# Kernel tuning notes

Measured on AMD Instinct MI355X. Metric: run time of the kernel, lower is better.

The kernel has to match this reference:

```python
import jax, jax.numpy as jnp
import numpy as np
import math

B, L, T, IN, H, DEPTH, HEADS = 4096, 1, 64, 16, 128, 3, 2
HD = H // HEADS
EPS = 1e-5


def layer_norm(x, g, b):
    u = jnp.mean(x, axis=-1, keepdims=True)
    s = jnp.mean((x - u) ** 2, axis=-1, keepdims=True)
    return g * (x - u) / jnp.sqrt(s + EPS) + b


def mlp(x, W, b, g, beta):
    return jax.nn.relu(layer_norm(x @ W + b, g, beta))


def attention(h, amask, Wq, bq, Wk, bk, Wv, bv):
    N, Tn, _ = h.shape
    def heads(x):
        return x.reshape(N, Tn, HEADS, HD).transpose(0, 2, 1, 3)
    q = heads(h @ Wq + bq)
    k = heads(h @ Wk + bk)
    v = heads(h @ Wv + bv)
    scores = jnp.einsum('nhqd,nhkd->nhqk', q, k) / math.sqrt(HD)
    scores = scores + (1.0 - amask[:, None]) * -10000.0
    probs = jax.nn.softmax(scores, axis=-1)
    ctx = jnp.einsum('nhqk,nhkd->nhqd', probs, v)
    return ctx.transpose(0, 2, 1, 3).reshape(N, Tn, H)


def setup_inputs() -> dict:
    key = jax.random.key(0)
    ks = jax.random.split(key, 8)
    feat = jax.random.normal(ks[0], (B, L, T, IN), jnp.float32)
    seq_lens = jax.random.randint(ks[1], (B, L), 1, T + 1)
    pos = jnp.arange(T)
    # repo convention: 0 = valid node, 1 = padded; prefix-valid layout
    masks = (pos[None, None, :] >= seq_lens[..., None]).astype(jnp.float32)[..., None]
    s = 0.02
    W_emb = jax.random.normal(ks[2], (IN, H), jnp.float32) * s
    W_enc = jax.random.normal(ks[3], (H, H), jnp.float32) * s
    Wq = jax.random.normal(ks[4], (DEPTH, H, H), jnp.float32) * s
    Wk = jax.random.normal(ks[5], (DEPTH, H, H), jnp.float32) * s
    Wv = jax.random.normal(ks[6], (DEPTH, H, H), jnp.float32) * s
    return dict(
        lane_nodes_feat=feat, masks=masks,
        W_emb=W_emb, b_emb=jnp.zeros((H,)), g_emb=jnp.ones((H,)), beta_emb=jnp.zeros((H,)),
        W_enc=W_enc, b_enc=jnp.zeros((H,)), g_enc=jnp.ones((H,)), beta_enc=jnp.zeros((H,)),
        Wq=Wq, bq=jnp.zeros((DEPTH, H)), Wk=Wk, bk=jnp.zeros((DEPTH, H)), Wv=Wv, bv=jnp.zeros((DEPTH, H)),
        ln_g=jnp.ones((DEPTH, H)), ln_b=jnp.zeros((DEPTH, H)),
    )


def reference(lane_nodes_feat, masks, W_emb, b_emb, g_emb, beta_emb, W_enc, b_enc,
              g_enc, beta_enc, Wq, bq, Wk, bk, Wv, bv, ln_g, ln_b):
    emb = mlp(lane_nodes_feat, W_emb, b_emb, g_emb, beta_emb)   # [B,L,T,H]
    emb = mlp(emb, W_enc, b_enc, g_enc, beta_enc)
    # every (b,l) lane has >=1 valid node by construction, so masked_select == reshape
    hs = emb.reshape(B * L, T, H)
    seq_lens = jnp.sum(1.0 - masks[:, :, :, 0], axis=-1).reshape(B * L)  # [N]
    pos = jnp.arange(T)
    valid = pos[None, :] < seq_lens[:, None]                              # [N,T]
    amask = (valid[:, :, None] & valid[:, None, :]).astype(hs.dtype)      # [N,T,T]
    for d in range(DEPTH):
        temp = hs
        hs = attention(hs, amask, Wq[d], bq[d], Wk[d], bk[d], Wv[d], bv[d])
        hs = jax.nn.relu(hs) + temp
        hs = layer_norm(hs, ln_g[d], ln_b[d])
    hs = jnp.max(hs, axis=1)                                              # [N,H]
    return hs.reshape(B, L, H)
```

## Files before the change

kernel.cpp:

```cpp
#include <hip/hip_runtime.h>

typedef unsigned short u16;
typedef unsigned int u32;
typedef __attribute__((ext_vector_type(8))) short short8;
typedef __attribute__((ext_vector_type(4))) float floatx4;

#define EPSV 1e-5f
#define WS_ELEMS 167936

__device__ __forceinline__ float b2f(u16 u){
  union { float f; u32 i; } c; c.i = ((u32)u) << 16; return c.f;
}
__device__ __forceinline__ u16 f2b(float f){
  union { float f; u32 i; } c; c.f = f;
  u32 r = c.i + 0x7FFFu + ((c.i >> 16) & 1u);
  return (u16)(r >> 16);
}
__device__ __forceinline__ u16 f2bc(float f){
  union { float f; u32 i; } c; c.f = f;
  return (u16)((c.i + 0x8000u) >> 16);
}
__device__ __forceinline__ float ldf(const void* p, int i, bool isf){
  return isf ? ((const float*)p)[i] : b2f(((const u16*)p)[i]);
}
__device__ __forceinline__ bool detect_f32(const void* g_emb){
  return *(const u32*)g_emb == 0x3F800000u;
}
__device__ __forceinline__ void dma16(const u16* g, u16* l){
  __builtin_amdgcn_global_load_lds((const __attribute__((address_space(1))) u32*)(g),
                                   (__attribute__((address_space(3))) u32*)(l), 16, 0, 0);
}
__device__ __forceinline__ void dma_slab(const u16* g, u16* dst, int wave, int lane){
  #pragma unroll
  for (int i = 0; i < 4; i++){
    int c = (wave << 2) + i;
    dma16(g + (c << 9) + (lane << 3), dst + (c << 9));
  }
}

__global__ void prep_kernel(const void* W_emb, const void* W_enc,
                            const void* Wq, const void* Wk, const void* Wv,
                            const void* g_emb, u16* ws){
  bool isf = detect_f32(g_emb);
  int e = blockIdx.x * 256 + threadIdx.x;
  if (e >= WS_ELEMS) return;
  float v;
  if (e < 4096){
    int half = e >> 11, r = e & 2047;
    int nt = r >> 9, q = (r >> 3) & 63, j = r & 7;
    int col = half*64 + nt*16 + (q & 15);
    int k = (q >> 4)*8 + j;
    v = (k < 16) ? ldf(W_emb, k*128 + col, isf) : 0.0f;
  } else if (e < 20480){
    int i = e - 4096;
    int half = i >> 13, r = i & 8191;
    int chunk = r >> 9, q = (r >> 3) & 63, j = r & 7;
    int ks = chunk >> 2, nt = chunk & 3;
    int col = half*64 + nt*16 + (q & 15);
    int k = ks*32 + (q >> 4)*8 + j;
    v = ldf(W_enc, k*128 + col, isf);
  } else {
    int i = e - 20480;
    int slab = i >> 13, r = i & 8191;
    int dh = slab / 3, which = slab - dh*3;
    int d = dh >> 1, h = dh & 1;
    int chunk = r >> 9, q = (r >> 3) & 63, j = r & 7;
    int ks = chunk >> 2, nt = chunk & 3;
    int col = h*64 + nt*16 + (q & 15);
    int k = ks*32 + (q >> 4)*8 + j;
    const void* W = (which == 0) ? Wv : (which == 1) ? Wk : Wq;
    v = ldf(W, d*16384 + k*128 + col, isf);
  }
  ws[e] = f2b(v);
}

__device__ __forceinline__ short8 frg(const u16* p, int chunk, int lane){
  return *(const short8*)(p + (chunk << 9) + (lane << 3));
}
__device__ __forceinline__ int wfoff(int wave, int nt, int lq, int lc){
  return ((((nt >> 1) << 2) + wave) << 9)
       + ((((((nt << 1) + (lc >> 3)) & 3) << 4) + (lq << 2)) << 3) + (lc & 7);
}
__device__ __forceinline__ int qfoff(int wave, int nt, int lq, int lc){
  return (wave << 10) + ((nt >> 1) << 9)
       + ((((((nt << 1) + (lc >> 3)) & 3) << 4) + (lq << 2)) << 3) + (lc & 7);
}

__device__ __forceinline__ void gemmW(const u16* sh, const u16* slab, int wave, int lane, floatx4* acc){
  #pragma unroll
  for (int ks = 0; ks < 4; ks++){
    short8 a = frg(sh, ks*4 + wave, lane);
    #pragma unroll
    for (int nt = 0; nt < 4; nt++)
      acc[nt] = __builtin_amdgcn_mfma_f32_16x16x32_bf16(a, frg(slab, ks*4 + nt, lane), acc[nt], 0, 0, 0);
  }
}
__device__ __forceinline__ void gemmWT(const u16* sh, const u16* slab, int wave, int lane, floatx4* acc){
  #pragma unroll
  for (int ks = 0; ks < 4; ks++){
    short8 a = frg(slab, ks*4 + wave, lane);
    #pragma unroll
    for (int nt = 0; nt < 4; nt++)
      acc[nt] = __builtin_amdgcn_mfma_f32_16x16x32_bf16(a, frg(sh, ks*4 + nt, lane), acc[nt], 0, 0, 0);
  }
}
__device__ __forceinline__ void gemm64(const u16* areg, const u16* b, int wave, int lane, floatx4* acc){
  #pragma unroll
  for (int ks = 0; ks < 2; ks++){
    short8 a = *(const short8*)(areg + (wave << 10) + (ks << 9) + (lane << 3));
    #pragma unroll
    for (int nt = 0; nt < 4; nt++)
      acc[nt] = __builtin_amdgcn_mfma_f32_16x16x32_bf16(a, frg(b, ks*4 + nt, lane), acc[nt], 0, 0, 0);
  }
}

__device__ __forceinline__ void red_sum2(float* s1, float* s2){
  #pragma unroll
  for (int m = 1; m < 16; m <<= 1){
    #pragma unroll
    for (int r = 0; r < 4; r++){
      s1[r] += __shfl_xor(s1[r], m, 64);
      s2[r] += __shfl_xor(s2[r], m, 64);
    }
  }
}

__device__ __forceinline__ void ln_mlp(floatx4* acc, const void* bias, const void* g,
    const void* bet, bool isf, float xres[8][4], int wave, int lq, int lc, u16* sh){
  float x[8][4], s1[4] = {0,0,0,0}, s2[4] = {0,0,0,0};
  #pragma unroll
  for (int nt = 0; nt < 8; nt++){
    float bb = ldf(bias, nt*16 + lc, isf);
    #pragma unroll
    for (int r = 0; r < 4; r++){
      float v = acc[nt][r] + bb;
      x[nt][r] = v; s1[r] += v; s2[r] += v*v;
    }
  }
  red_sum2(s1, s2);
  float mean[4], rstd[4];
  #pragma unroll
  for (int r = 0; r < 4; r++){
    mean[r] = s1[r] * (1.0f/128.0f);
    rstd[r] = rsqrtf(s2[r]*(1.0f/128.0f) - mean[r]*mean[r] + EPSV);
  }
  #pragma unroll
  for (int nt = 0; nt < 8; nt++){
    float gg = ldf(g, nt*16 + lc, isf), bb = ldf(bet, nt*16 + lc, isf);
    int o = wfoff(wave, nt, lq, lc);
    #pragma unroll
    for (int r = 0; r < 4; r++){
      float y = fmaxf((x[nt][r] - mean[r]) * rstd[r] * gg + bb, 0.0f);
      xres[nt][r] = y;
      sh[o + 8*r] = f2bc(y);
    }
  }
}

__device__ __forceinline__ void ln_attn(floatx4* ctx, float xres[8][4], const u16* cb,
                                        int wave, int lq, int lc, u16* sh){
  float x[8][4], s1[4] = {0,0,0,0}, s2[4] = {0,0,0,0};
  #pragma unroll
  for (int nt = 0; nt < 8; nt++){
    #pragma unroll
    for (int r = 0; r < 4; r++){
      float v = fmaxf(ctx[nt][r], 0.0f) + xres[nt][r];
      x[nt][r] = v; s1[r] += v; s2[r] += v*v;
    }
  }
  red_sum2(s1, s2);
  float mean[4], rstd[4];
  #pragma unroll
  for (int r = 0; r < 4; r++){
    mean[r] = s1[r] * (1.0f/128.0f);
    rstd[r] = rsqrtf(s2[r]*(1.0f/128.0f) - mean[r]*mean[r] + EPSV);
  }
  #pragma unroll
  for (int nt = 0; nt < 8; nt++){
    float gg = b2f(cb[384 + nt*16 + lc]), bb = b2f(cb[512 + nt*16 + lc]);
    int o = wfoff(wave, nt, lq, lc);
    #pragma unroll
    for (int r = 0; r < 4; r++){
      float y = (x[nt][r] - mean[r]) * rstd[r] * gg + bb;
      xres[nt][r] = y;
      sh[o + 8*r] = f2bc(y);
    }
  }
}

__global__ __launch_bounds__(256, 3)
void fused_kernel(const void* feat, const void* masks,
                  const void* b_emb, const void* g_emb, const void* be_emb,
                  const void* b_enc, const void* g_enc, const void* be_enc,
                  const void* bq, const void* bk, const void* bv,
                  const void* ln_g, const void* ln_b,
                  const u16* ws, void* out){
  __shared__ __align__(16) u16 s_h[8192];
  __shared__ __align__(16) u16 s_w[8192];
  __shared__ __align__(16) u16 s_k[4096];
  __shared__ __align__(16) u16 s_v[4096];
  __shared__ u16 s_c[1920];
  __shared__ float s_valid[64];

  int tid = threadIdx.x;
  int wave = tid >> 6, lane = tid & 63, lq = lane >> 4, lc = lane & 15;
  int n = blockIdx.x;
  bool isf = detect_f32(g_emb);
  const floatx4 z4 = {0.0f, 0.0f, 0.0f, 0.0f};

  dma16(ws + ((wave*2 + 0) << 9) + (lane << 3), s_w + ((wave*2 + 0) << 9));
  dma16(ws + ((wave*2 + 1) << 9) + (lane << 3), s_w + ((wave*2 + 1) << 9));

  if (!isf){
    const u16* fp = (const u16*)feat + n*1024;
    if (tid < 128){
      int t = tid >> 1, half = tid & 1;
      uint4 v = *(const uint4*)(fp + t*16 + half*8);
      *(uint4*)(s_h + ((t >> 4) << 9) + (((half << 4) + (t & 15)) << 3)) = v;
    } else {
      int t = (tid - 128) >> 1, half = 2 + ((tid - 128) & 1);
      uint4 z; z.x = 0; z.y = 0; z.z = 0; z.w = 0;
      *(uint4*)(s_h + ((t >> 4) << 9) + (((half << 4) + (t & 15)) << 3)) = z;
    }
  } else {
    for (int i = tid; i < 2048; i += 256){
      int t = i >> 5, k = i & 31;
      float v = (k < 16) ? ((const float*)feat)[n*1024 + t*16 + k] : 0.0f;
      s_h[((t >> 4) << 9) + ((((k >> 3) << 4) + (t & 15)) << 3) + (k & 7)] = f2b(v);
    }
  }
  for (int i = tid; i < 1920; i += 256){
    int blk = i >> 7, off = i & 127;
    int d = blk / 5, wh = blk - d*5;
    const void* src = (wh == 0) ? bq : (wh == 1) ? bk : (wh == 2) ? bv : (wh == 3) ? ln_g : ln_b;
    s_c[i] = isf ? f2b(((const float*)src)[d*128 + off]) : ((const u16*)src)[d*128 + off];
  }
  if (tid < 64) s_valid[tid] = (ldf(masks, n*64 + tid, isf) == 0.0f) ? 1.0f : 0.0f;
  __syncthreads();

  float xres[8][4];
  floatx4 acc[8];
  #pragma unroll
  for (int i = 0; i < 8; i++) acc[i] = z4;
  {
    short8 a = frg(s_h, wave, lane);
    #pragma unroll
    for (int nt = 0; nt < 4; nt++){
      acc[nt]     = __builtin_amdgcn_mfma_f32_16x16x32_bf16(a, frg(s_w, nt,     lane), acc[nt],     0,0,0);
      acc[4 + nt] = __builtin_amdgcn_mfma_f32_16x16x32_bf16(a, frg(s_w, 4 + nt, lane), acc[4 + nt], 0,0,0);
    }
  }
  __syncthreads();
  dma_slab(ws + 4096, s_w, wave, lane);
  ln_mlp(acc, b_emb, g_emb, be_emb, isf, xres, wave, lq, lc, s_h);
  __syncthreads();

  #pragma unroll
  for (int i = 0; i < 8; i++) acc[i] = z4;
  gemmW(s_h, s_w, wave, lane, acc);
  __syncthreads();
  dma_slab(ws + 12288, s_w, wave, lane);
  __syncthreads();
  gemmW(s_h, s_w, wave, lane, acc + 4);
  __syncthreads();
  dma_slab(ws + 20480, s_w, wave, lane);
  ln_mlp(acc, b_enc, g_enc, be_enc, isf, xres, wave, lq, lc, s_h);
  __syncthreads();

  int sb = 20480;
  for (int d = 0; d < 3; d++){
    const u16* cb = s_c + d*640;
    floatx4 ctx[8];
    #pragma unroll
    for (int i = 0; i < 8; i++) ctx[i] = z4;

    for (int h = 0; h < 2; h++){
      floatx4 pa[4];
      #pragma unroll
      for (int i = 0; i < 4; i++) pa[i] = z4;
      gemmWT(s_h, s_w, wave, lane, pa);
      __syncthreads();
      dma_slab(ws + sb + 8192, s_w, wave, lane);
      {
        float bb4[4];
        #pragma unroll
        for (int r = 0; r < 4; r++) bb4[r] = b2f(cb[256 + h*64 + wave*16 + (lq << 2) + r]);
        #pragma unroll
        for (int nt = 0; nt < 4; nt++){
          int o = wfoff(wave, nt, lq, lc);
          #pragma unroll
          for (int r = 0; r < 4; r++) s_v[o + 8*r] = f2bc(pa[nt][r] + bb4[r]);
        }
      }
      __syncthreads();
      #pragma unroll
      for (int i = 0; i < 4; i++) pa[i] = z4;
      gemmW(s_h, s_w, wave, lane, pa);
      __syncthreads();
      dma_slab(ws + sb + 16384, s_w, wave, lane);
      {
        #pragma unroll
        for (int nt = 0; nt < 4; nt++){
          float bb = b2f(cb[128 + h*64 + nt*16 + lc]);
          int o = wfoff(wave, nt, lq, lc);
          #pragma unroll
          for (int r = 0; r < 4; r++) s_k[o + 8*r] = f2bc(pa[nt][r] + bb);
        }
      }
      __syncthreads();
      #pragma unroll
      for (int i = 0; i < 4; i++) pa[i] = z4;
      gemmW(s_h, s_w, wave, lane, pa);
      __syncthreads();
      {
        #pragma unroll
        for (int nt = 0; nt < 4; nt++){
          float bb = b2f(cb[h*64 + nt*16 + lc]);
          int o = qfoff(wave, nt, lq, lc);
          #pragma unroll
          for (int r = 0; r < 4; r++) s_w[o + 8*r] = f2bc(pa[nt][r] + bb);
        }
      }
      #pragma unroll
      for (int i = 0; i < 4; i++) pa[i] = z4;
      gemm64(s_w, s_k, wave, lane, pa);

      float rv[4], cv[4];
      #pragma unroll
      for (int r = 0; r < 4; r++) rv[r] = s_valid[wave*16 + (lq << 2) + r];
      #pragma unroll
      for (int nt = 0; nt < 4; nt++) cv[nt] = s_valid[nt*16 + lc];

      float p[4][4];
      #pragma unroll
      for (int nt = 0; nt < 4; nt++)
        #pragma unroll
        for (int r = 0; r < 4; r++)
          p[nt][r] = pa[nt][r]*0.125f - 10000.0f*(1.0f - rv[r]*cv[nt]);

      float mx[4];
      #pragma unroll
      for (int r = 0; r < 4; r++)
        mx[r] = fmaxf(fmaxf(p[0][r], p[1][r]), fmaxf(p[2][r], p[3][r]));
      #pragma unroll
      for (int m = 1; m < 16; m <<= 1)
        #pragma unroll
        for (int r = 0; r < 4; r++) mx[r] = fmaxf(mx[r], __shfl_xor(mx[r], m, 64));

      float sm[4] = {0,0,0,0};
      #pragma unroll
      for (int nt = 0; nt < 4; nt++)
        #pragma unroll
        for (int r = 0; r < 4; r++){ p[nt][r] = __expf(p[nt][r] - mx[r]); sm[r] += p[nt][r]; }
      #pragma unroll
      for (int m = 1; m < 16; m <<= 1)
        #pragma unroll
        for (int r = 0; r < 4; r++) sm[r] += __shfl_xor(sm[r], m, 64);

      float inv[4];
      #pragma unroll
      for (int r = 0; r < 4; r++) inv[r] = 1.0f / sm[r];

      #pragma unroll
      for (int nt = 0; nt < 4; nt++){
        int o = qfoff(wave, nt, lq, lc);
        #pragma unroll
        for (int r = 0; r < 4; r++) s_w[o + 8*r] = f2bc(p[nt][r] * inv[r]);
      }
      gemm64(s_w, s_v, wave, lane, ctx + h*4);
      __syncthreads();
      sb += 24576;
      if (!(d == 2 && h == 1)) dma_slab(ws + sb, s_w, wave, lane);
      if (h == 1) ln_attn(ctx, xres, cb, wave, lq, lc, s_h);
      __syncthreads();
    }
  }

  if (tid < 128){
    int col = tid;
    float mxv = -1e30f;
    #pragma unroll 4
    for (int t = 0; t < 64; t++)
      mxv = fmaxf(mxv, b2f(s_h[((((col >> 5) << 2) + (t >> 4)) << 9)
                               + (((((col >> 3) & 3) << 4) + (t & 15)) << 3) + (col & 7)]));
    if (isf) ((float*)out)[n*128 + col] = mxv;
    else     ((u16*)out)[n*128 + col] = f2b(mxv);
  }
}

extern "C" void kernel_launch(void* const* d_in, const int* in_sizes, int n_in,
                              void* d_out, int out_size, void* d_ws, size_t ws_size,
                              hipStream_t stream){
  const void* feat   = d_in[0];
  const void* masks  = d_in[1];
  const void* W_emb  = d_in[2];
  const void* b_emb  = d_in[3];
  const void* g_emb  = d_in[4];
  const void* be_emb = d_in[5];
  const void* W_enc  = d_in[6];
  const void* b_enc  = d_in[7];
  const void* g_enc  = d_in[8];
  const void* be_enc = d_in[9];
  const void* Wq     = d_in[10];
  const void* bq     = d_in[11];
  const void* Wk     = d_in[12];
  const void* bk     = d_in[13];
  const void* Wv     = d_in[14];
  const void* bv     = d_in[15];
  const void* ln_g   = d_in[16];
  const void* ln_b   = d_in[17];
  u16* ws = (u16*)d_ws;

  hipLaunchKernelGGL(prep_kernel, dim3((WS_ELEMS + 255)/256), dim3(256), 0, stream,
                     W_emb, W_enc, Wq, Wk, Wv, g_emb, ws);
  hipLaunchKernelGGL(fused_kernel, dim3(4096), dim3(256), 0, stream,
                     feat, masks, b_emb, g_emb, be_emb, b_enc, g_enc, be_enc,
                     bq, bk, bv, ln_g, ln_b, ws, d_out);
}
```

Measured before the change: 383.3 us.

## Transpose MLP GEMMs, drop register residual, pack bf16 stores, split final max

The two MLP GEMMs now use swapped MFMA operands, so each lane holds four consecutive feature columns of one token. LayerNorm then reduces with two cross-lane shuffles and writes packed bf16 via v_cvt_pk_bf16_f32 as 8-byte stores. The 32-float residual array kept in registers is removed, and the residual is reread from the bf16 copy in LDS, aiming to lower register pressure at some precision cost. The final max-pool uses all 256 threads with a shuffle combine, and may_alias types plus compiler memory barriers are added for the type-punned LDS accesses.

```diff
diff --git a/kernel.cpp b/kernel.cpp
--- a/kernel.cpp
+++ b/kernel.cpp
@@ -2,11 +2,18 @@
 
 typedef unsigned short u16;
 typedef unsigned int u32;
-typedef __attribute__((ext_vector_type(8))) short short8;
+typedef __attribute__((ext_vector_type(8))) short short8_;
+typedef short8_ short8 __attribute__((may_alias));
+typedef __attribute__((ext_vector_type(4))) short short4v_;
+typedef short4v_ short4v __attribute__((may_alias));
+typedef uint4 uint4a __attribute__((may_alias));
+typedef ushort4 ushort4a __attribute__((may_alias));
+typedef float4 float4a __attribute__((may_alias));
 typedef __attribute__((ext_vector_type(4))) float floatx4;
 
 #define EPSV 1e-5f
 #define WS_ELEMS 167936
+#define MEMBAR() asm volatile("" ::: "memory")
 
 __device__ __forceinline__ float b2f(u16 u){
   union { float f; u32 i; } c; c.i = ((u32)u) << 16; return c.f;
@@ -20,8 +27,17 @@
   union { float f; u32 i; } c; c.f = f;
   return (u16)((c.i + 0x8000u) >> 16);
 }
+__device__ __forceinline__ u32 pkbf(float lo, float hi){
+  u32 r; asm("v_cvt_pk_bf16_f32 %0, %1, %2" : "=v"(r) : "v"(lo), "v"(hi));
+  return r;
+}
 __device__ __forceinline__ float ldf(const void* p, int i, bool isf){
   return isf ? ((const float*)p)[i] : b2f(((const u16*)p)[i]);
+}
+__device__ __forceinline__ float4 ldf4(const void* p, int i4, bool isf){
+  if (isf) return ((const float4a*)p)[i4];
+  ushort4 u = ((const ushort4a*)p)[i4];
+  return make_float4(b2f(u.x), b2f(u.y), b2f(u.z), b2f(u.w));
 }
 __device__ __forceinline__ bool detect_f32(const void* g_emb){
   return *(const u32*)g_emb == 0x3F800000u;
@@ -77,6 +93,15 @@
 __device__ __forceinline__ short8 frg(const u16* p, int chunk, int lane){
   return *(const short8*)(p + (chunk << 9) + (lane << 3));
 }
+__device__ __forceinline__ void wr4(u16* dst, int off, float v0, float v1, float v2, float v3){
+  union { u32 w[2]; short4v s; } u;
+  u.w[0] = pkbf(v0, v1); u.w[1] = pkbf(v2, v3);
+  *(short4v*)(dst + off) = u.s;
+}
+__device__ __forceinline__ int toff(int wave, int nt, int lq, int lc){
+  return ((((nt >> 1) << 2) + wave) << 9)
+       + ((((((nt & 1) << 1) + (lq >> 1)) << 4) + lc) << 3) + ((lq & 1) << 2);
+}
 __device__ __forceinline__ int wfoff(int wave, int nt, int lq, int lc){
   return ((((nt >> 1) << 2) + wave) << 9)
        + ((((((nt << 1) + (lc >> 3)) & 3) << 4) + (lq << 2)) << 3) + (lc & 7);
@@ -104,6 +129,15 @@
       acc[nt] = __builtin_amdgcn_mfma_f32_16x16x32_bf16(a, frg(sh, ks*4 + nt, lane), acc[nt], 0, 0, 0);
   }
 }
+__device__ __forceinline__ void gemmT(const u16* slab, const u16* sh, int wave, int lane, floatx4* acc){
+  #pragma unroll
+  for (int ks = 0; ks < 4; ks++){
+    short8 b = frg(sh, ks*4 + wave, lane);
+    #pragma unroll
+    for (int nt = 0; nt < 4; nt++)
+      acc[nt] = __builtin_amdgcn_mfma_f32_16x16x32_bf16(frg(slab, ks*4 + nt, lane), b, acc[nt], 0, 0, 0);
+  }
+}
 __device__ __forceinline__ void gemm64(const u16* areg, const u16* b, int wave, int lane, floatx4* acc){
   #pragma unroll
   for (int ks = 0; ks < 2; ks++){
@@ -125,18 +159,46 @@
   }
 }
 
-__device__ __forceinline__ void ln_mlp(floatx4* acc, const void* bias, const void* g,
-    const void* bet, bool isf, float xres[8][4], int wave, int lq, int lc, u16* sh){
+__device__ __forceinline__ void ln_mlp_T(floatx4* acc, const void* bias, const void* g,
+    const void* bet, bool isf, int wave, int lq, int lc, u16* sh){
+  float x[8][4]; float s1 = 0.0f, s2 = 0.0f;
+  #pragma unroll
+  for (int nt = 0; nt < 8; nt++){
+    float4 bb = ldf4(bias, nt*4 + lq, isf);
+    float v0 = acc[nt][0] + bb.x, v1 = acc[nt][1] + bb.y;
+    float v2 = acc[nt][2] + bb.z, v3 = acc[nt][3] + bb.w;
+    x[nt][0]=v0; x[nt][1]=v1; x[nt][2]=v2; x[nt][3]=v3;
+    s1 += (v0+v1) + (v2+v3);
+    s2 += (v0*v0+v1*v1) + (v2*v2+v3*v3);
+  }
+  s1 += __shfl_xor(s1, 16, 64); s2 += __shfl_xor(s2, 16, 64);
+  s1 += __shfl_xor(s1, 32, 64); s2 += __shfl_xor(s2, 32, 64);
+  float mean = s1 * (1.0f/128.0f);
+  float rstd = rsqrtf(s2*(1.0f/128.0f) - mean*mean + EPSV);
+  #pragma unroll
+  for (int nt = 0; nt < 8; nt++){
+    float4 gg = ldf4(g, nt*4 + lq, isf), bb = ldf4(bet, nt*4 + lq, isf);
+    float y0 = fmaxf((x[nt][0]-mean)*rstd*gg.x + bb.x, 0.0f);
+    float y1 = fmaxf((x[nt][1]-mean)*rstd*gg.y + bb.y, 0.0f);
+    float y2 = fmaxf((x[nt][2]-mean)*rstd*gg.z + bb.z, 0.0f);
+    float y3 = fmaxf((x[nt][3]-mean)*rstd*gg.w + bb.w, 0.0f);
+    wr4(sh, toff(wave, nt, lq, lc), y0, y1, y2, y3);
+  }
+}
+
+__device__ __forceinline__ void ln_attn_res(floatx4* ctx, const u16* cb,
+                                            int wave, int lq, int lc, u16* sh){
   float x[8][4], s1[4] = {0,0,0,0}, s2[4] = {0,0,0,0};
   #pragma unroll
   for (int nt = 0; nt < 8; nt++){
-    float bb = ldf(bias, nt*16 + lc, isf);
+    int o = wfoff(wave, nt, lq, lc);
     #pragma unroll
     for (int r = 0; r < 4; r++){
-      float v = acc[nt][r] + bb;
+      float v = fmaxf(ctx[nt][r], 0.0f) + b2f(sh[o + 8*r]);
       x[nt][r] = v; s1[r] += v; s2[r] += v*v;
     }
   }
+  MEMBAR();
   red_sum2(s1, s2);
   float mean[4], rstd[4];
   #pragma unroll
@@ -146,43 +208,11 @@
   }
   #pragma unroll
   for (int nt = 0; nt < 8; nt++){
-    float gg = ldf(g, nt*16 + lc, isf), bb = ldf(bet, nt*16 + lc, isf);
-    int o = wfoff(wave, nt, lq, lc);
-    #pragma unroll
-    for (int r = 0; r < 4; r++){
-      float y = fmaxf((x[nt][r] - mean[r]) * rstd[r] * gg + bb, 0.0f);
-      xres[nt][r] = y;
-      sh[o + 8*r] = f2bc(y);
-    }
-  }
-}
-
-__device__ __forceinline__ void ln_attn(floatx4* ctx, float xres[8][4], const u16* cb,
-                                        int wave, int lq, int lc, u16* sh){
-  float x[8][4], s1[4] = {0,0,0,0}, s2[4] = {0,0,0,0};
-  #pragma unroll
-  for (int nt = 0; nt < 8; nt++){
-    #pragma unroll
-    for (int r = 0; r < 4; r++){
-      float v = fmaxf(ctx[nt][r], 0.0f) + xres[nt][r];
-      x[nt][r] = v; s1[r] += v; s2[r] += v*v;
-    }
-  }
-  red_sum2(s1, s2);
-  float mean[4], rstd[4];
-  #pragma unroll
-  for (int r = 0; r < 4; r++){
-    mean[r] = s1[r] * (1.0f/128.0f);
-    rstd[r] = rsqrtf(s2[r]*(1.0f/128.0f) - mean[r]*mean[r] + EPSV);
-  }
-  #pragma unroll
-  for (int nt = 0; nt < 8; nt++){
     float gg = b2f(cb[384 + nt*16 + lc]), bb = b2f(cb[512 + nt*16 + lc]);
     int o = wfoff(wave, nt, lq, lc);
     #pragma unroll
     for (int r = 0; r < 4; r++){
       float y = (x[nt][r] - mean[r]) * rstd[r] * gg + bb;
-      xres[nt][r] = y;
       sh[o + 8*r] = f2bc(y);
     }
   }
@@ -199,8 +229,8 @@
   __shared__ __align__(16) u16 s_w[8192];
   __shared__ __align__(16) u16 s_k[4096];
   __shared__ __align__(16) u16 s_v[4096];
-  __shared__ u16 s_c[1920];
-  __shared__ float s_valid[64];
+  __shared__ __align__(16) u16 s_c[1920];
+  __shared__ __align__(16) float s_valid[64];
 
   int tid = threadIdx.x;
   int wave = tid >> 6, lane = tid & 63, lq = lane >> 4, lc = lane & 15;
@@ -215,12 +245,12 @@
     const u16* fp = (const u16*)feat + n*1024;
     if (tid < 128){
       int t = tid >> 1, half = tid & 1;
-      uint4 v = *(const uint4*)(fp + t*16 + half*8);
-      *(uint4*)(s_h + ((t >> 4) << 9) + (((half << 4) + (t & 15)) << 3)) = v;
+      uint4 v = *(const uint4a*)(fp + t*16 + half*8);
+      *(uint4a*)(s_h + ((t >> 4) << 9) + (((half << 4) + (t & 15)) << 3)) = v;
     } else {
       int t = (tid - 128) >> 1, half = 2 + ((tid - 128) & 1);
       uint4 z; z.x = 0; z.y = 0; z.z = 0; z.w = 0;
-      *(uint4*)(s_h + ((t >> 4) << 9) + (((half << 4) + (t & 15)) << 3)) = z;
+      *(uint4a*)(s_h + ((t >> 4) << 9) + (((half << 4) + (t & 15)) << 3)) = z;
     }
   } else {
     for (int i = tid; i < 2048; i += 256){
@@ -238,33 +268,30 @@
   if (tid < 64) s_valid[tid] = (ldf(masks, n*64 + tid, isf) == 0.0f) ? 1.0f : 0.0f;
   __syncthreads();
 
-  float xres[8][4];
   floatx4 acc[8];
   #pragma unroll
   for (int i = 0; i < 8; i++) acc[i] = z4;
   {
-    short8 a = frg(s_h, wave, lane);
-    #pragma unroll
-    for (int nt = 0; nt < 4; nt++){
-      acc[nt]     = __builtin_amdgcn_mfma_f32_16x16x32_bf16(a, frg(s_w, nt,     lane), acc[nt],     0,0,0);
-      acc[4 + nt] = __builtin_amdgcn_mfma_f32_16x16x32_bf16(a, frg(s_w, 4 + nt, lane), acc[4 + nt], 0,0,0);
-    }
+    short8 b = frg(s_h, wave, lane);
+    #pragma unroll
+    for (int nt = 0; nt < 8; nt++)
+      acc[nt] = __builtin_amdgcn_mfma_f32_16x16x32_bf16(frg(s_w, nt, lane), b, acc[nt], 0, 0, 0);
   }
   __syncthreads();
   dma_slab(ws + 4096, s_w, wave, lane);
-  ln_mlp(acc, b_emb, g_emb, be_emb, isf, xres, wave, lq, lc, s_h);
+  ln_mlp_T(acc, b_emb, g_emb, be_emb, isf, wave, lq, lc, s_h);
   __syncthreads();
 
   #pragma unroll
   for (int i = 0; i < 8; i++) acc[i] = z4;
-  gemmW(s_h, s_w, wave, lane, acc);
+  gemmT(s_w, s_h, wave, lane, acc);
   __syncthreads();
   dma_slab(ws + 12288, s_w, wave, lane);
   __syncthreads();
-  gemmW(s_h, s_w, wave, lane, acc + 4);
+  gemmT(s_w, s_h, wave, lane, acc + 4);
   __syncthreads();
   dma_slab(ws + 20480, s_w, wave, lane);
-  ln_mlp(acc, b_enc, g_enc, be_enc, isf, xres, wave, lq, lc, s_h);
+  ln_mlp_T(acc, b_enc, g_enc, be_enc, isf, wave, lq, lc, s_h);
   __syncthreads();
 
   int sb = 20480;
@@ -321,6 +348,7 @@
           for (int r = 0; r < 4; r++) s_w[o + 8*r] = f2bc(pa[nt][r] + bb);
         }
       }
+      MEMBAR();
       #pragma unroll
       for (int i = 0; i < 4; i++) pa[i] = z4;
       gemm64(s_w, s_k, wave, lane, pa);
@@ -367,24 +395,32 @@
         #pragma unroll
         for (int r = 0; r < 4; r++) s_w[o + 8*r] = f2bc(p[nt][r] * inv[r]);
       }
+      MEMBAR();
       gemm64(s_w, s_v, wave, lane, ctx + h*4);
       __syncthreads();
       sb += 24576;
       if (!(d == 2 && h == 1)) dma_slab(ws + sb, s_w, wave, lane);
-      if (h == 1) ln_attn(ctx, xres, cb, wave, lq, lc, s_h);
-      __syncthreads();
-    }
-  }
-
-  if (tid < 128){
-    int col = tid;
+      if (h == 1) ln_attn_res(ctx, cb, wave, lq, lc, s_h);
+      __syncthreads();
+    }
+  }
+
+  {
+    int col = tid >> 1, th = tid & 1;
+    int base = ((col >> 5) << 2);
+    int lp = (((col >> 3) & 3) << 4);
+    int jj = col & 7;
     float mxv = -1e30f;
-    #pragma unroll 4
-    for (int t = 0; t < 64; t++)
-      mxv = fmaxf(mxv, b2f(s_h[((((col >> 5) << 2) + (t >> 4)) << 9)
-                               + (((((col >> 3) & 3) << 4) + (t & 15)) << 3) + (col & 7)]));
-    if (isf) ((float*)out)[n*128 + col] = mxv;
-    else     ((u16*)out)[n*128 + col] = f2b(mxv);
+    #pragma unroll 8
+    for (int t = 0; t < 32; t++){
+      int tt = (th << 5) + t;
+      mxv = fmaxf(mxv, b2f(s_h[((base + (tt >> 4)) << 9) + ((lp + (tt & 15)) << 3) + jj]));
+    }
+    mxv = fmaxf(mxv, __shfl_xor(mxv, 1, 64));
+    if (!th){
+      if (isf) ((float*)out)[n*128 + col] = mxv;
+      else     ((u16*)out)[n*128 + col]  = f2b(mxv);
+    }
   }
 }
 
```

Result: slower. 472.0 us (+23.2%).
